# Kernel optimization log

Measured on AMD Instinct MI355X. Metric: run time of the kernel, lower is better.

Reference implementation:

```python
import jax, jax.numpy as jnp
import numpy as np

H = 8            # num_heads
SIM_THRESH = 0.75


def setup_inputs() -> dict:
    key = jax.random.key(0)
    ks = jax.random.split(key, 6)
    B, N, C, CR = 1, 1536, 256, 64
    x_cls = jax.random.normal(ks[0], (B, N, C), dtype=jnp.float32)
    x_reg = jax.random.normal(ks[1], (B, N, CR), dtype=jnp.float32)
    cls_score = jax.random.uniform(ks[2], (N,), dtype=jnp.float32)
    fg_score = jax.random.uniform(ks[3], (1, 1, 1, N), dtype=jnp.float32)
    W_cls = jax.random.normal(ks[4], (C, 3 * C), dtype=jnp.float32) / np.sqrt(C).astype(np.float32)
    W_reg = jax.random.normal(ks[5], (CR, 3 * CR), dtype=jnp.float32) / np.sqrt(CR).astype(np.float32)
    return {"x_cls": x_cls, "x_reg": x_reg, "cls_score": cls_score,
            "fg_score": fg_score, "W_cls": W_cls, "W_reg": W_reg}


def _l2norm(t):
    return t / jnp.linalg.norm(t, axis=-1, keepdims=True)


def _split_qkv(x, W):
    B, N, C = x.shape
    qkv = (x @ W).reshape(B, N, 3, H, C // H).transpose(2, 0, 3, 1, 4)  # [3,B,H,N,hd]
    return qkv[0], qkv[1], qkv[2]


def reference(x_cls, x_reg, cls_score, fg_score, W_cls, W_reg):
    B, N, C = x_cls.shape
    CR = x_reg.shape[-1]
    scale = (C // H) ** -0.5  # note: torch code uses the cls head_dim scale for BOTH branches

    q, k, v = _split_qkv(x_cls, W_cls)
    qn, kn, vn = _l2norm(q), _l2norm(k), _l2norm(v)
    qr, kr, vr = _split_qkv(x_reg, W_reg)
    qrn, krn, vrn = _l2norm(qr), _l2norm(kr), _l2norm(vr)

    # cls_score broadcast: value cls_score[j] at position (i, j), as in torch's reshape+repeat
    cs = cls_score.reshape(1, 1, 1, N)
    cls_mask = (cs > jnp.swapaxes(cs, -2, -1) - 0.1).astype(jnp.float32)        # [1,1,N,N]
    fg_mask = (fg_score > jnp.swapaxes(fg_score, -2, -1) - 0.1).astype(jnp.float32)  # [1,1,N,N]

    # raw cosine-similarity matrices of the (normalized) value vectors
    attn_cls_raw = jnp.einsum('bhid,bhjd->bhij', vn, vn)   # [B,H,N,N]
    attn_reg_raw = jnp.einsum('bhid,bhjd->bhij', vrn, vrn)

    attn_cls = jax.nn.softmax(
        jnp.einsum('bhid,bhjd->bhij', qn, kn) * scale * cs * cls_mask, axis=-1)
    attn_reg = jax.nn.softmax(
        jnp.einsum('bhid,bhjd->bhij', qrn, krn) * scale, axis=-1)
    attn = (attn_cls + attn_reg) * 0.5

    # threshold masks (mask=True, use_mask=True, sim_thresh=0.75 defaults)
    sim_mask = (attn_cls_raw.mean(axis=1) > SIM_THRESH).astype(jnp.float32)    # [B,N,N]
    sim_mask = jnp.broadcast_to(sim_mask[:, None], (B, H, N, N))
    sim_mask = sim_mask * cls_mask[0, 0] * fg_mask[0, 0]
    obj_mask = (attn_reg_raw.mean(axis=1)[0] > SIM_THRESH).astype(jnp.float32)  # [N,N]

    attn = sim_mask * attn
    obj_mask = obj_mask * sim_mask                                   # [B,H,N,N]
    obj_mask = obj_mask / jnp.sum(obj_mask, axis=-1, keepdims=True)  # safe: diagonal always 1
    attn = obj_mask * attn

    x = jnp.einsum('bhij,bhjd->bhid', attn, v).transpose(0, 2, 1, 3).reshape(B, N, C)
    out_cls = jnp.concatenate([x, x_cls], axis=-1)                   # [B,N,2C]
    xr = jnp.einsum('bhij,bhjd->bhid', attn, vr).transpose(0, 2, 1, 3).reshape(B, N, CR)
    out_reg = jnp.concatenate([xr, x_reg], axis=-1)                  # [B,N,2*CR]
    return out_cls, out_reg, sim_mask, obj_mask
```

## Files before the change

kernel.cpp:

```cpp
#include <hip/hip_runtime.h>
#include <hip/hip_bf16.h>

#define NT 1536
#define SCALE 0.17677669529663687f

typedef __attribute__((ext_vector_type(8))) short bf16x8;
typedef __attribute__((ext_vector_type(4))) float f32x4;

static __device__ __forceinline__ unsigned short f2b(float x) {
    __hip_bfloat16 h = __float2bfloat16(x);
    union { __hip_bfloat16 b; unsigned short u; } cv; cv.b = h; return cv.u;
}
static __device__ __forceinline__ float b2f(unsigned short u) {
    union { float f; unsigned v; } c; c.v = ((unsigned)u) << 16; return c.f;
}

__global__ __launch_bounds__(256) void prep(
    const float* __restrict__ x_cls, const float* __restrict__ x_reg,
    const float* __restrict__ W_cls, const float* __restrict__ W_reg,
    unsigned short* __restrict__ xb_c, unsigned short* __restrict__ xb_r,
    unsigned short* __restrict__ Wt_c, unsigned short* __restrict__ Wt_r)
{
    const int u = blockIdx.x * 256 + threadIdx.x;
    if (u < 393216) {
        xb_c[u] = f2b(x_cls[u]);
    } else if (u < 491520) {
        const int v = u - 393216;
        xb_r[v] = f2b(x_reg[v]);
    } else if (u < 688128) {
        const int v = u - 491520;
        const int j = v >> 8, k = v & 255;
        Wt_c[v] = f2b(W_cls[k * 768 + j]);
    } else if (u < 700416) {
        const int v = u - 688128;
        const int j = v >> 6, k = v & 63;
        Wt_r[v] = f2b(W_reg[k * 192 + j]);
    }
}

__global__ __launch_bounds__(256) void gemm_mfma(
    const unsigned short* __restrict__ xb_c, const unsigned short* __restrict__ Wt_c,
    const unsigned short* __restrict__ xb_r, const unsigned short* __restrict__ Wt_r,
    float* __restrict__ qkv_c, unsigned short* __restrict__ qb_c,
    float* __restrict__ qkv_r, unsigned short* __restrict__ qb_r)
{
    const unsigned short *A, *B;
    float* qkv; unsigned short* qb;
    int K, NN, KS;
    const bool isreg = (blockIdx.z == 1);
    if (!isreg) { A = xb_c; B = Wt_c; qkv = qkv_c; qb = qb_c; K = 256; NN = 768; KS = 8; }
    else { if (blockIdx.x >= 3) return;
           A = xb_r; B = Wt_r; qkv = qkv_r; qb = qb_r; K = 64;  NN = 192; KS = 2; }
    __shared__ short Ai[64 * 40], Bj[64 * 40];
    const int t = threadIdx.x, lane = t & 63;
    const int wv = t >> 6, wr = wv >> 1, wc = wv & 1;
    const int i0 = blockIdx.y * 64, j0 = blockIdx.x * 64;
    const int srow = t >> 2, sc8 = (t & 3) * 8;
    f32x4 acc[2][2];
    #pragma unroll
    for (int a = 0; a < 2; a++)
        #pragma unroll
        for (int b = 0; b < 2; b++) acc[a][b] = (f32x4){0, 0, 0, 0};
    float4 ra = *(const float4*)&A[(i0 + srow) * K + 0 * 32 + sc8];
    float4 rb = *(const float4*)&B[(j0 + srow) * K + 0 * 32 + sc8];
    float4 ra2, rb2;
    if (KS > 1) {
        ra2 = *(const float4*)&A[(i0 + srow) * K + 1 * 32 + sc8];
        rb2 = *(const float4*)&B[(j0 + srow) * K + 1 * 32 + sc8];
    }
    for (int ks = 0; ks < KS; ks++) {
        __syncthreads();
        *(float4*)&Ai[srow * 40 + sc8] = ra;
        *(float4*)&Bj[srow * 40 + sc8] = rb;
        ra = ra2; rb = rb2;
        if (ks + 2 < KS) {
            ra2 = *(const float4*)&A[(i0 + srow) * K + (ks + 2) * 32 + sc8];
            rb2 = *(const float4*)&B[(j0 + srow) * K + (ks + 2) * 32 + sc8];
        }
        __syncthreads();
        const int k8 = (lane >> 4) * 8;
        bf16x8 af[2], bf_[2];
        #pragma unroll
        for (int fr = 0; fr < 2; fr++)
            af[fr] = *(const bf16x8*)&Ai[(wr * 32 + fr * 16 + (lane & 15)) * 40 + k8];
        #pragma unroll
        for (int fc = 0; fc < 2; fc++)
            bf_[fc] = *(const bf16x8*)&Bj[(wc * 32 + fc * 16 + (lane & 15)) * 40 + k8];
        #pragma unroll
        for (int fr = 0; fr < 2; fr++)
            #pragma unroll
            for (int fc = 0; fc < 2; fc++)
                acc[fr][fc] = __builtin_amdgcn_mfma_f32_16x16x32_bf16(af[fr], bf_[fc], acc[fr][fc], 0, 0, 0);
    }
    #pragma unroll
    for (int fr = 0; fr < 2; fr++)
        #pragma unroll
        for (int r4 = 0; r4 < 4; r4++) {
            const int i = i0 + wr * 32 + fr * 16 + (lane >> 4) * 4 + r4;
            if (!isreg) {
                float s = acc[fr][0][r4] * acc[fr][0][r4] + acc[fr][1][r4] * acc[fr][1][r4];
                s += __shfl_xor(s, 1); s += __shfl_xor(s, 2);
                s += __shfl_xor(s, 4); s += __shfl_xor(s, 8);
                const float inv = 1.0f / sqrtf(s);
                #pragma unroll
                for (int fc = 0; fc < 2; fc++) {
                    const int j = j0 + wc * 32 + fc * 16 + (lane & 15);
                    const float v = acc[fr][fc][r4];
                    qkv[i * NN + j] = v;
                    qb[i * NN + j] = f2b(v * inv);
                }
            } else {
                #pragma unroll
                for (int fc = 0; fc < 2; fc++) {
                    const float v = acc[fr][fc][r4];
                    float s = v * v;
                    s += __shfl_xor(s, 1); s += __shfl_xor(s, 2); s += __shfl_xor(s, 4);
                    const float inv = 1.0f / sqrtf(s);
                    const int j = j0 + wc * 32 + fc * 16 + (lane & 15);
                    qkv[i * NN + j] = v;
                    qb[i * NN + j] = f2b(v * inv);
                }
            }
        }
}

__global__ __launch_bounds__(256) void bitsdenom(
    const unsigned short* __restrict__ qb_cls, const unsigned short* __restrict__ qb_reg,
    const float* __restrict__ cls_score, const float* __restrict__ fg_score,
    unsigned* __restrict__ simbits, unsigned* __restrict__ objbits,
    float* __restrict__ Dcpart, float* __restrict__ Drpart)
{
    __shared__ short Ai[64 * 40], Bj[64 * 40];
    __shared__ short Kr[64 * 72], Qr[64 * 72];
    __shared__ float csi[64], csj[64], fgi[64], fgj[64];
    __shared__ unsigned simw[64][2], objw[64][2];
    const int t = threadIdx.x;
    const int lane = t & 63;
    const int wv = t >> 6, wr = wv >> 1, wc = wv & 1;
    const int sr = t >> 2, sc = t & 3;

    if (blockIdx.x < 576) {
        const int iB = blockIdx.x / 24, jB = blockIdx.x % 24;
        const int i0 = iB * 64, j0 = jB * 64;
        if (t < 64)       { csi[t] = cls_score[i0 + t]; fgi[t] = fg_score[i0 + t]; }
        else if (t < 128) { csj[t - 64] = cls_score[j0 + t - 64]; fgj[t - 64] = fg_score[j0 + t - 64]; }
        f32x4 ac[2][2], ar[2][2];
        #pragma unroll
        for (int a = 0; a < 2; a++)
            #pragma unroll
            for (int b = 0; b < 2; b++) { ac[a][b] = (f32x4){0,0,0,0}; ar[a][b] = (f32x4){0,0,0,0}; }
        #define LD_A(s) ((s) < 8 ? *(const float4*)&qb_cls[(i0 + sr) * 768 + 512 + (s) * 32 + sc * 8] \
                                 : *(const float4*)&qb_reg[(i0 + sr) * 192 + 128 + ((s) - 8) * 32 + sc * 8])
        #define LD_B(s) ((s) < 8 ? *(const float4*)&qb_cls[(j0 + sr) * 768 + 512 + (s) * 32 + sc * 8] \
                                 : *(const float4*)&qb_reg[(j0 + sr) * 192 + 128 + ((s) - 8) * 32 + sc * 8])
        float4 ra = LD_A(0), rb = LD_B(0);
        float4 ra2 = LD_A(1), rb2 = LD_B(1);
        for (int ks = 0; ks < 10; ks++) {
            __syncthreads();
            *(float4*)&Ai[sr * 40 + sc * 8] = ra;
            *(float4*)&Bj[sr * 40 + sc * 8] = rb;
            ra = ra2; rb = rb2;
            if (ks + 2 < 10) { ra2 = LD_A(ks + 2); rb2 = LD_B(ks + 2); }
            __syncthreads();
            const int k8 = (lane >> 4) * 8;
            bf16x8 af[2], bf_[2];
            #pragma unroll
            for (int fr = 0; fr < 2; fr++)
                af[fr] = *(const bf16x8*)&Ai[(wr * 32 + fr * 16 + (lane & 15)) * 40 + k8];
            #pragma unroll
            for (int fc = 0; fc < 2; fc++)
                bf_[fc] = *(const bf16x8*)&Bj[(wc * 32 + fc * 16 + (lane & 15)) * 40 + k8];
            if (ks < 8) {
                #pragma unroll
                for (int fr = 0; fr < 2; fr++)
                    #pragma unroll
                    for (int fc = 0; fc < 2; fc++)
                        ac[fr][fc] = __builtin_amdgcn_mfma_f32_16x16x32_bf16(af[fr], bf_[fc], ac[fr][fc], 0, 0, 0);
            } else {
                #pragma unroll
                for (int fr = 0; fr < 2; fr++)
                    #pragma unroll
                    for (int fc = 0; fc < 2; fc++)
                        ar[fr][fc] = __builtin_amdgcn_mfma_f32_16x16x32_bf16(af[fr], bf_[fc], ar[fr][fc], 0, 0, 0);
            }
        }
        #undef LD_A
        #undef LD_B
        #pragma unroll
        for (int fr = 0; fr < 2; fr++)
            #pragma unroll
            for (int r4 = 0; r4 < 4; r4++) {
                const int rloc = wr * 32 + fr * 16 + (lane >> 4) * 4 + r4;
                const float ci = csi[rloc] - 0.1f, fgv = fgi[rloc] - 0.1f;
                unsigned sm[2], om[2];
                #pragma unroll
                for (int fc = 0; fc < 2; fc++) {
                    const int cloc = wc * 32 + fc * 16 + (lane & 15);
                    const bool clsb = csj[cloc] > ci;
                    const bool fgb  = fgj[cloc] > fgv;
                    const bool sim = (ac[fr][fc][r4] * 0.125f > 0.75f) && clsb && fgb;
                    const bool obj = sim && (ar[fr][fc][r4] * 0.125f > 0.75f);
                    unsigned long long bs = __ballot(sim);
                    unsigned long long bo = __ballot(obj);
                    const int g = lane >> 4;
                    sm[fc] = (unsigned)((bs >> (16 * g)) & 0xFFFFull);
                    om[fc] = (unsigned)((bo >> (16 * g)) & 0xFFFFull);
                }
                if ((lane & 15) == 0) {
                    simw[rloc][wc] = sm[0] | (sm[1] << 16);
                    objw[rloc][wc] = om[0] | (om[1] << 16);
                }
            }
        __syncthreads();
        if (t < 128) {
            const int row = t >> 1, w = t & 1;
            simbits[(i0 + row) * 48 + jB * 2 + w] = simw[row][w];
            objbits[(i0 + row) * 48 + jB * 2 + w] = objw[row][w];
        }
    } else {
        const int vd = blockIdx.x - 576;
        const int iB = vd / 24, jB = vd % 24;
        const int i0 = iB * 64, j0 = jB * 64;
        if (t < 64)       csj[t] = cls_score[j0 + t];
        else if (t < 128) csi[t - 64] = cls_score[i0 + t - 64];
        #pragma unroll
        for (int it = 0; it < 2; it++) {
            const int u = it * 256 + t;
            const int r = u >> 3, c = u & 7;
            *(float4*)&Kr[r * 72 + c * 8] = *(const float4*)&qb_reg[(j0 + r) * 192 + 64 + c * 8];
            *(float4*)&Qr[r * 72 + c * 8] = *(const float4*)&qb_reg[(i0 + r) * 192 + 0 + c * 8];
        }
        __syncthreads();
        float cI[2], cJ[8];
        #pragma unroll
        for (int fc = 0; fc < 2; fc++) cI[fc] = csi[wc * 32 + fc * 16 + (lane & 15)] - 0.1f;
        #pragma unroll
        for (int fr = 0; fr < 2; fr++)
            #pragma unroll
            for (int r4 = 0; r4 < 4; r4++)
                cJ[fr * 4 + r4] = csj[wr * 32 + fr * 16 + (lane >> 4) * 4 + r4];
        float pC[2][8], pR[2][8];
        const bool g0 = (lane >> 4) == 0;
        const bf16x8 zz = {0, 0, 0, 0, 0, 0, 0, 0};
        float4 ra = *(const float4*)&qb_cls[(j0 + sr) * 768 + 256 + 0 * 32 + sc * 8];
        float4 rb = *(const float4*)&qb_cls[(i0 + sr) * 768 + 0   + 0 * 32 + sc * 8];
        float4 ra2 = *(const float4*)&qb_cls[(j0 + sr) * 768 + 256 + 1 * 32 + sc * 8];
        float4 rb2 = *(const float4*)&qb_cls[(i0 + sr) * 768 + 0   + 1 * 32 + sc * 8];
        for (int h = 0; h < 8; h++) {
            __syncthreads();
            *(float4*)&Ai[sr * 40 + sc * 8] = ra;
            *(float4*)&Bj[sr * 40 + sc * 8] = rb;
            ra = ra2; rb = rb2;
            if (h + 2 < 8) {
                ra2 = *(const float4*)&qb_cls[(j0 + sr) * 768 + 256 + (h + 2) * 32 + sc * 8];
                rb2 = *(const float4*)&qb_cls[(i0 + sr) * 768 + 0   + (h + 2) * 32 + sc * 8];
            }
            __syncthreads();
            const int k8 = (lane >> 4) * 8;
            bf16x8 a[2], b[2], arg[2], brg[2];
            #pragma unroll
            for (int fr = 0; fr < 2; fr++) {
                const int row = wr * 32 + fr * 16 + (lane & 15);
                a[fr] = *(const bf16x8*)&Ai[row * 40 + k8];
                arg[fr] = g0 ? *(const bf16x8*)&Kr[row * 72 + h * 8] : zz;
            }
            #pragma unroll
            for (int fc = 0; fc < 2; fc++) {
                const int row = wc * 32 + fc * 16 + (lane & 15);
                b[fc] = *(const bf16x8*)&Bj[row * 40 + k8];
                brg[fc] = g0 ? *(const bf16x8*)&Qr[row * 72 + h * 8] : zz;
            }
            f32x4 acc[2][2], racc[2][2];
            #pragma unroll
            for (int fr = 0; fr < 2; fr++)
                #pragma unroll
                for (int fc = 0; fc < 2; fc++) {
                    acc[fr][fc] = (f32x4){0,0,0,0};
                    racc[fr][fc] = (f32x4){0,0,0,0};
                    acc[fr][fc] = __builtin_amdgcn_mfma_f32_16x16x32_bf16(a[fr], b[fc], acc[fr][fc], 0, 0, 0);
                    racc[fr][fc] = __builtin_amdgcn_mfma_f32_16x16x32_bf16(arg[fr], brg[fc], racc[fr][fc], 0, 0, 0);
                }
            #pragma unroll
            for (int fc = 0; fc < 2; fc++) {
                float sC = 0.f, sR = 0.f;
                #pragma unroll
                for (int fr = 0; fr < 2; fr++)
                    #pragma unroll
                    for (int r4 = 0; r4 < 4; r4++) {
                        const float cj = cJ[fr * 4 + r4];
                        const float lc = (cj > cI[fc]) ? acc[fr][fc][r4] * SCALE * cj : 0.0f;
                        sC += __expf(lc);
                        sR += __expf(racc[fr][fc][r4] * SCALE);
                    }
                pC[fc][h] = sC; pR[fc][h] = sR;
            }
        }
        #pragma unroll
        for (int fc = 0; fc < 2; fc++)
            #pragma unroll
            for (int h = 0; h < 8; h++) {
                float v = pC[fc][h]; v += __shfl_xor(v, 16); v += __shfl_xor(v, 32);
                float u = pR[fc][h]; u += __shfl_xor(u, 16); u += __shfl_xor(u, 32);
                if (lane < 16) {
                    const int i = i0 + wc * 32 + fc * 16 + lane;
                    const int p = jB * 2 + wr;
                    Dcpart[(p * NT + i) * 8 + h] = v;
                    Drpart[(p * NT + i) * 8 + h] = u;
                }
            }
    }
}

__global__ __launch_bounds__(256) void finish(
    const float* __restrict__ qkv_cls, const unsigned short* __restrict__ qb_cls,
    const float* __restrict__ qkv_reg, const unsigned short* __restrict__ qb_reg,
    const float* __restrict__ cls_score,
    const unsigned* __restrict__ simbits, const unsigned* __restrict__ objbits,
    const float* __restrict__ Dcpart, const float* __restrict__ Drpart,
    const float* __restrict__ x_cls, const float* __restrict__ x_reg,
    float* __restrict__ out_cls, float* __restrict__ out_reg,
    float* __restrict__ sim_out, float* __restrict__ obj_out)
{
    __shared__ unsigned bw[6][48];
    __shared__ float invs[6];
    const int t = threadIdx.x;
    if (blockIdx.x < 384) {
        const int i = (blockIdx.x << 2) + (t >> 6);
        const int l = t & 63;
        const int g = l >> 3;
        const ushort4 qu = *(const ushort4*)&qb_cls[i * 768 + 4 * l];
        const float qx = b2f(qu.x), qy = b2f(qu.y), qz = b2f(qu.z), qw = b2f(qu.w);
        const float qr = b2f(qb_reg[i * 192 + l]);
        unsigned myw = (l < 48) ? objbits[i * 48 + l] : 0u;
        int cnt = __popc(myw);
        #pragma unroll
        for (int m = 1; m < 64; m <<= 1) cnt += __shfl_xor(cnt, m);
        const int s = l & 7;
        float Dcv = 0.f, Drv = 0.f;
        #pragma unroll
        for (int p6 = 0; p6 < 6; p6++) {
            const int p = s * 6 + p6;
            Dcv += Dcpart[(p * NT + i) * 8 + g];
            Drv += Drpart[(p * NT + i) * 8 + g];
        }
        Dcv += __shfl_xor(Dcv, 1); Dcv += __shfl_xor(Dcv, 2); Dcv += __shfl_xor(Dcv, 4);
        Drv += __shfl_xor(Drv, 1); Drv += __shfl_xor(Drv, 2); Drv += __shfl_xor(Drv, 4);
        float a1x = 0.f, a1y = 0.f, a1z = 0.f, a1w = 0.f;
        float a2x = 0.f, a2y = 0.f, a2z = 0.f, a2w = 0.f;
        float rr1 = 0.f, rr2 = 0.f;
        for (int w = 0; w < 48; w++) {
            unsigned bits = __shfl(myw, w);
            while (bits) {
                const int b = __ffs(bits) - 1;
                bits &= bits - 1u;
                const int j = w * 32 + b;
                const ushort4 ku = *(const ushort4*)&qb_cls[j * 768 + 256 + 4 * l];
                const float4 v4 = *(const float4*)&qkv_cls[j * 768 + 512 + 4 * l];
                const float kr = b2f(qb_reg[j * 192 + 64 + l]);
                const float vr = qkv_reg[j * 192 + 128 + l];
                float dc = qx * b2f(ku.x) + qy * b2f(ku.y) + qz * b2f(ku.z) + qw * b2f(ku.w);
                dc += __shfl_xor(dc, 1); dc += __shfl_xor(dc, 2); dc += __shfl_xor(dc, 4);
                float dr = qr * kr;
                dr += __shfl_xor(dr, 1); dr += __shfl_xor(dr, 2); dr += __shfl_xor(dr, 4);
                const float cj = cls_score[j];
                const float ec = __expf(dc * SCALE * cj);
                const float er = __expf(dr * SCALE);
                a1x += ec * v4.x; a1y += ec * v4.y; a1z += ec * v4.z; a1w += ec * v4.w;
                a2x += er * v4.x; a2y += er * v4.y; a2z += er * v4.z; a2w += er * v4.w;
                rr1 += ec * vr;   rr2 += er * vr;
            }
        }
        const float iDc = 1.0f / Dcv, iDr = 1.0f / Drv;
        const float hi = 0.5f / (float)cnt;
        float4 o;
        o.x = (a1x * iDc + a2x * iDr) * hi;
        o.y = (a1y * iDc + a2y * iDr) * hi;
        o.z = (a1z * iDc + a2z * iDr) * hi;
        o.w = (a1w * iDc + a2w * iDr) * hi;
        *(float4*)&out_cls[i * 512 + 4 * l] = o;
        out_reg[i * 128 + l] = (rr1 * iDc + rr2 * iDr) * hi;
        *(float4*)&out_cls[i * 512 + 256 + 4 * l] = *(const float4*)&x_cls[i * 256 + 4 * l];
        out_reg[i * 128 + 64 + l] = x_reg[i * 64 + l];
    } else {
        const int eb = blockIdx.x - 384;
        const int arr = eb >> 11;
        const int rem = eb & 2047;
        const int copy = rem >> 8;
        const int blk = rem & 255;
        const int r0 = blk * 6;
        const unsigned* src = arr ? objbits : simbits;
        for (int u = t; u < 288; u += 256) bw[u / 48][u % 48] = src[(r0 + u / 48) * 48 + (u % 48)];
        __syncthreads();
        if (t < 6) {
            int c = 0;
            #pragma unroll 8
            for (int w = 0; w < 48; w++) c += __popc(bw[t][w]);
            invs[t] = 1.0f / (float)c;
        }
        __syncthreads();
        f32x4* dst = (f32x4*)((arr ? obj_out : sim_out)
                              + (size_t)copy * NT * NT + (size_t)r0 * NT);
        #pragma unroll
        for (int rpt = 0; rpt < 9; rpt++) {
            const int u = rpt * 256 + t;
            const int row = u / 384;
            const int c4 = u - row * 384;
            const int j0 = c4 * 4;
            const unsigned w = bw[row][j0 >> 5] >> (j0 & 31);
            const float on = arr ? invs[row] : 1.0f;
            f32x4 v;
            v.x = (w & 1u) ? on : 0.f;
            v.y = (w & 2u) ? on : 0.f;
            v.z = (w & 4u) ? on : 0.f;
            v.w = (w & 8u) ? on : 0.f;
            __builtin_nontemporal_store(v, dst + u);
        }
    }
}

extern "C" void kernel_launch(void* const* d_in, const int* in_sizes, int n_in,
                              void* d_out, int out_size, void* d_ws, size_t ws_size,
                              hipStream_t stream)
{
    (void)in_sizes; (void)n_in; (void)out_size; (void)ws_size;
    const float* x_cls     = (const float*)d_in[0];
    const float* x_reg     = (const float*)d_in[1];
    const float* cls_score = (const float*)d_in[2];
    const float* fg_score  = (const float*)d_in[3];
    const float* W_cls     = (const float*)d_in[4];
    const float* W_reg     = (const float*)d_in[5];

    float* out = (float*)d_out;
    float* out_cls = out;
    float* out_reg = out + 786432;
    float* sim_out = out + 983040;
    float* obj_out = out + 19857408;

    float* wsf = (float*)d_ws;
    float* qkv_cls = wsf;
    float* qkv_reg = wsf + 1179648;
    float* Dcpart  = wsf + 1474560;
    float* Drpart  = wsf + 2064384;
    unsigned short* qb_cls = (unsigned short*)(wsf + 2654208);
    unsigned short* qb_reg = (unsigned short*)(wsf + 3244032);
    unsigned short* xb_c   = (unsigned short*)(wsf + 3391488);
    unsigned short* xb_r   = (unsigned short*)(wsf + 3588096);
    unsigned short* Wt_c   = (unsigned short*)(wsf + 3637248);
    unsigned short* Wt_r   = (unsigned short*)(wsf + 3735552);
    unsigned* simbits = (unsigned*)(wsf + 3741696);
    unsigned* objbits = simbits + 73728;

    prep<<<2736, 256, 0, stream>>>(x_cls, x_reg, W_cls, W_reg, xb_c, xb_r, Wt_c, Wt_r);
    gemm_mfma<<<dim3(12, 24, 2), 256, 0, stream>>>(
        xb_c, Wt_c, xb_r, Wt_r, qkv_cls, qb_cls, qkv_reg, qb_reg);
    bitsdenom<<<1152, 256, 0, stream>>>(
        qb_cls, qb_reg, cls_score, fg_score, simbits, objbits, Dcpart, Drpart);
    finish<<<4480, 256, 0, stream>>>(
        qkv_cls, qb_cls, qkv_reg, qb_reg, cls_score,
        simbits, objbits, Dcpart, Drpart, x_cls, x_reg,
        out_cls, out_reg, sim_out, obj_out);
}
```

Measured before the change: 81.84 us.

## Regroup kernels so denominator blocks interleave with mask expansion stores

Splits the bitmask MFMA pass into its own kernel. The softmax-denominator blocks now share a launch with the large sim/obj mask expansion, interleaved one denominator block per seven expansion blocks, and the sparse attention output moves to a separate final kernel. The intent is to overlap the compute-bound denominator work with the store-bound writing of the 2x8xNxN masks instead of running them in separate phases. It adds one kernel launch and makes the denominator blocks depend on the masks being finished.

Measured after the change: 169.9 us. 108% more time.

```diff
diff --git a/kernel.cpp b/kernel.cpp
--- a/kernel.cpp
+++ b/kernel.cpp
@@ -124,103 +124,119 @@
         }
 }
 
-__global__ __launch_bounds__(256) void bitsdenom(
+__global__ __launch_bounds__(256) void bits_mfma(
     const unsigned short* __restrict__ qb_cls, const unsigned short* __restrict__ qb_reg,
     const float* __restrict__ cls_score, const float* __restrict__ fg_score,
-    unsigned* __restrict__ simbits, unsigned* __restrict__ objbits,
-    float* __restrict__ Dcpart, float* __restrict__ Drpart)
+    unsigned* __restrict__ simbits, unsigned* __restrict__ objbits)
 {
     __shared__ short Ai[64 * 40], Bj[64 * 40];
-    __shared__ short Kr[64 * 72], Qr[64 * 72];
     __shared__ float csi[64], csj[64], fgi[64], fgj[64];
     __shared__ unsigned simw[64][2], objw[64][2];
     const int t = threadIdx.x;
     const int lane = t & 63;
     const int wv = t >> 6, wr = wv >> 1, wc = wv & 1;
     const int sr = t >> 2, sc = t & 3;
-
-    if (blockIdx.x < 576) {
-        const int iB = blockIdx.x / 24, jB = blockIdx.x % 24;
+    const int iB = blockIdx.x / 24, jB = blockIdx.x % 24;
+    const int i0 = iB * 64, j0 = jB * 64;
+    if (t < 64)       { csi[t] = cls_score[i0 + t]; fgi[t] = fg_score[i0 + t]; }
+    else if (t < 128) { csj[t - 64] = cls_score[j0 + t - 64]; fgj[t - 64] = fg_score[j0 + t - 64]; }
+    f32x4 ac[2][2], ar[2][2];
+    #pragma unroll
+    for (int a = 0; a < 2; a++)
+        #pragma unroll
+        for (int b = 0; b < 2; b++) { ac[a][b] = (f32x4){0,0,0,0}; ar[a][b] = (f32x4){0,0,0,0}; }
+    #define LD_A(s) ((s) < 8 ? *(const float4*)&qb_cls[(i0 + sr) * 768 + 512 + (s) * 32 + sc * 8] \
+                             : *(const float4*)&qb_reg[(i0 + sr) * 192 + 128 + ((s) - 8) * 32 + sc * 8])
+    #define LD_B(s) ((s) < 8 ? *(const float4*)&qb_cls[(j0 + sr) * 768 + 512 + (s) * 32 + sc * 8] \
+                             : *(const float4*)&qb_reg[(j0 + sr) * 192 + 128 + ((s) - 8) * 32 + sc * 8])
+    float4 ra = LD_A(0), rb = LD_B(0);
+    float4 ra2 = LD_A(1), rb2 = LD_B(1);
+    for (int ks = 0; ks < 10; ks++) {
+        __syncthreads();
+        *(float4*)&Ai[sr * 40 + sc * 8] = ra;
+        *(float4*)&Bj[sr * 40 + sc * 8] = rb;
+        ra = ra2; rb = rb2;
+        if (ks + 2 < 10) { ra2 = LD_A(ks + 2); rb2 = LD_B(ks + 2); }
+        __syncthreads();
+        const int k8 = (lane >> 4) * 8;
+        bf16x8 af[2], bf_[2];
+        #pragma unroll
+        for (int fr = 0; fr < 2; fr++)
+            af[fr] = *(const bf16x8*)&Ai[(wr * 32 + fr * 16 + (lane & 15)) * 40 + k8];
+        #pragma unroll
+        for (int fc = 0; fc < 2; fc++)
+            bf_[fc] = *(const bf16x8*)&Bj[(wc * 32 + fc * 16 + (lane & 15)) * 40 + k8];
+        if (ks < 8) {
+            #pragma unroll
+            for (int fr = 0; fr < 2; fr++)
+                #pragma unroll
+                for (int fc = 0; fc < 2; fc++)
+                    ac[fr][fc] = __builtin_amdgcn_mfma_f32_16x16x32_bf16(af[fr], bf_[fc], ac[fr][fc], 0, 0, 0);
+        } else {
+            #pragma unroll
+            for (int fr = 0; fr < 2; fr++)
+                #pragma unroll
+                for (int fc = 0; fc < 2; fc++)
+                    ar[fr][fc] = __builtin_amdgcn_mfma_f32_16x16x32_bf16(af[fr], bf_[fc], ar[fr][fc], 0, 0, 0);
+        }
+    }
+    #undef LD_A
+    #undef LD_B
+    #pragma unroll
+    for (int fr = 0; fr < 2; fr++)
+        #pragma unroll
+        for (int r4 = 0; r4 < 4; r4++) {
+            const int rloc = wr * 32 + fr * 16 + (lane >> 4) * 4 + r4;
+            const float ci = csi[rloc] - 0.1f, fgv = fgi[rloc] - 0.1f;
+            unsigned sm[2], om[2];
+            #pragma unroll
+            for (int fc = 0; fc < 2; fc++) {
+                const int cloc = wc * 32 + fc * 16 + (lane & 15);
+                const bool clsb = csj[cloc] > ci;
+                const bool fgb  = fgj[cloc] > fgv;
+                const bool sim = (ac[fr][fc][r4] * 0.125f > 0.75f) && clsb && fgb;
+                const bool obj = sim && (ar[fr][fc][r4] * 0.125f > 0.75f);
+                unsigned long long bs = __ballot(sim);
+                unsigned long long bo = __ballot(obj);
+                const int g = lane >> 4;
+                sm[fc] = (unsigned)((bs >> (16 * g)) & 0xFFFFull);
+                om[fc] = (unsigned)((bo >> (16 * g)) & 0xFFFFull);
+            }
+            if ((lane & 15) == 0) {
+                simw[rloc][wc] = sm[0] | (sm[1] << 16);
+                objw[rloc][wc] = om[0] | (om[1] << 16);
+            }
+        }
+    __syncthreads();
+    if (t < 128) {
+        const int row = t >> 1, w = t & 1;
+        simbits[(i0 + row) * 48 + jB * 2 + w] = simw[row][w];
+        objbits[(i0 + row) * 48 + jB * 2 + w] = objw[row][w];
+    }
+}
+
+__global__ __launch_bounds__(256) void denomexpand(
+    const unsigned short* __restrict__ qb_cls, const unsigned short* __restrict__ qb_reg,
+    const float* __restrict__ cls_score,
+    const unsigned* __restrict__ simbits, const unsigned* __restrict__ objbits,
+    float* __restrict__ Dcpart, float* __restrict__ Drpart,
+    float* __restrict__ sim_out, float* __restrict__ obj_out)
+{
+    __shared__ short Ai[64 * 40], Bj[64 * 40];
+    __shared__ short Kr[64 * 72], Qr[64 * 72];
+    __shared__ float csi[64], csj[64];
+    __shared__ unsigned bw[6][48];
+    __shared__ float invs[6];
+    const int t = threadIdx.x;
+    const int bid = blockIdx.x;
+    if ((bid & 7) == 7) {
+        const int didx = bid >> 3;
+        if (didx >= 576) return;
+        const int iB = didx / 24, jB = didx % 24;
         const int i0 = iB * 64, j0 = jB * 64;
-        if (t < 64)       { csi[t] = cls_score[i0 + t]; fgi[t] = fg_score[i0 + t]; }
-        else if (t < 128) { csj[t - 64] = cls_score[j0 + t - 64]; fgj[t - 64] = fg_score[j0 + t - 64]; }
-        f32x4 ac[2][2], ar[2][2];
-        #pragma unroll
-        for (int a = 0; a < 2; a++)
-            #pragma unroll
-            for (int b = 0; b < 2; b++) { ac[a][b] = (f32x4){0,0,0,0}; ar[a][b] = (f32x4){0,0,0,0}; }
-        #define LD_A(s) ((s) < 8 ? *(const float4*)&qb_cls[(i0 + sr) * 768 + 512 + (s) * 32 + sc * 8] \
-                                 : *(const float4*)&qb_reg[(i0 + sr) * 192 + 128 + ((s) - 8) * 32 + sc * 8])
-        #define LD_B(s) ((s) < 8 ? *(const float4*)&qb_cls[(j0 + sr) * 768 + 512 + (s) * 32 + sc * 8] \
-                                 : *(const float4*)&qb_reg[(j0 + sr) * 192 + 128 + ((s) - 8) * 32 + sc * 8])
-        float4 ra = LD_A(0), rb = LD_B(0);
-        float4 ra2 = LD_A(1), rb2 = LD_B(1);
-        for (int ks = 0; ks < 10; ks++) {
-            __syncthreads();
-            *(float4*)&Ai[sr * 40 + sc * 8] = ra;
-            *(float4*)&Bj[sr * 40 + sc * 8] = rb;
-            ra = ra2; rb = rb2;
-            if (ks + 2 < 10) { ra2 = LD_A(ks + 2); rb2 = LD_B(ks + 2); }
-            __syncthreads();
-            const int k8 = (lane >> 4) * 8;
-            bf16x8 af[2], bf_[2];
-            #pragma unroll
-            for (int fr = 0; fr < 2; fr++)
-                af[fr] = *(const bf16x8*)&Ai[(wr * 32 + fr * 16 + (lane & 15)) * 40 + k8];
-            #pragma unroll
-            for (int fc = 0; fc < 2; fc++)
-                bf_[fc] = *(const bf16x8*)&Bj[(wc * 32 + fc * 16 + (lane & 15)) * 40 + k8];
-            if (ks < 8) {
-                #pragma unroll
-                for (int fr = 0; fr < 2; fr++)
-                    #pragma unroll
-                    for (int fc = 0; fc < 2; fc++)
-                        ac[fr][fc] = __builtin_amdgcn_mfma_f32_16x16x32_bf16(af[fr], bf_[fc], ac[fr][fc], 0, 0, 0);
-            } else {
-                #pragma unroll
-                for (int fr = 0; fr < 2; fr++)
-                    #pragma unroll
-                    for (int fc = 0; fc < 2; fc++)
-                        ar[fr][fc] = __builtin_amdgcn_mfma_f32_16x16x32_bf16(af[fr], bf_[fc], ar[fr][fc], 0, 0, 0);
-            }
-        }
-        #undef LD_A
-        #undef LD_B
-        #pragma unroll
-        for (int fr = 0; fr < 2; fr++)
-            #pragma unroll
-            for (int r4 = 0; r4 < 4; r4++) {
-                const int rloc = wr * 32 + fr * 16 + (lane >> 4) * 4 + r4;
-                const float ci = csi[rloc] - 0.1f, fgv = fgi[rloc] - 0.1f;
-                unsigned sm[2], om[2];
-                #pragma unroll
-                for (int fc = 0; fc < 2; fc++) {
-                    const int cloc = wc * 32 + fc * 16 + (lane & 15);
-                    const bool clsb = csj[cloc] > ci;
-                    const bool fgb  = fgj[cloc] > fgv;
-                    const bool sim = (ac[fr][fc][r4] * 0.125f > 0.75f) && clsb && fgb;
-                    const bool obj = sim && (ar[fr][fc][r4] * 0.125f > 0.75f);
-                    unsigned long long bs = __ballot(sim);
-                    unsigned long long bo = __ballot(obj);
-                    const int g = lane >> 4;
-                    sm[fc] = (unsigned)((bs >> (16 * g)) & 0xFFFFull);
-                    om[fc] = (unsigned)((bo >> (16 * g)) & 0xFFFFull);
-                }
-                if ((lane & 15) == 0) {
-                    simw[rloc][wc] = sm[0] | (sm[1] << 16);
-                    objw[rloc][wc] = om[0] | (om[1] << 16);
-                }
-            }
-        __syncthreads();
-        if (t < 128) {
-            const int row = t >> 1, w = t & 1;
-            simbits[(i0 + row) * 48 + jB * 2 + w] = simw[row][w];
-            objbits[(i0 + row) * 48 + jB * 2 + w] = objw[row][w];
-        }
-    } else {
-        const int vd = blockIdx.x - 576;
-        const int iB = vd / 24, jB = vd % 24;
-        const int i0 = iB * 64, j0 = jB * 64;
+        const int lane = t & 63;
+        const int wv = t >> 6, wr = wv >> 1, wc = wv & 1;
+        const int sr = t >> 2, sc = t & 3;
         if (t < 64)       csj[t] = cls_score[j0 + t];
         else if (t < 128) csi[t - 64] = cls_score[i0 + t - 64];
         #pragma unroll
@@ -308,83 +324,11 @@
                     Drpart[(p * NT + i) * 8 + h] = u;
                 }
             }
-    }
-}
-
-__global__ __launch_bounds__(256) void finish(
-    const float* __restrict__ qkv_cls, const unsigned short* __restrict__ qb_cls,
-    const float* __restrict__ qkv_reg, const unsigned short* __restrict__ qb_reg,
-    const float* __restrict__ cls_score,
-    const unsigned* __restrict__ simbits, const unsigned* __restrict__ objbits,
-    const float* __restrict__ Dcpart, const float* __restrict__ Drpart,
-    const float* __restrict__ x_cls, const float* __restrict__ x_reg,
-    float* __restrict__ out_cls, float* __restrict__ out_reg,
-    float* __restrict__ sim_out, float* __restrict__ obj_out)
-{
-    __shared__ unsigned bw[6][48];
-    __shared__ float invs[6];
-    const int t = threadIdx.x;
-    if (blockIdx.x < 384) {
-        const int i = (blockIdx.x << 2) + (t >> 6);
-        const int l = t & 63;
-        const int g = l >> 3;
-        const ushort4 qu = *(const ushort4*)&qb_cls[i * 768 + 4 * l];
-        const float qx = b2f(qu.x), qy = b2f(qu.y), qz = b2f(qu.z), qw = b2f(qu.w);
-        const float qr = b2f(qb_reg[i * 192 + l]);
-        unsigned myw = (l < 48) ? objbits[i * 48 + l] : 0u;
-        int cnt = __popc(myw);
-        #pragma unroll
-        for (int m = 1; m < 64; m <<= 1) cnt += __shfl_xor(cnt, m);
-        const int s = l & 7;
-        float Dcv = 0.f, Drv = 0.f;
-        #pragma unroll
-        for (int p6 = 0; p6 < 6; p6++) {
-            const int p = s * 6 + p6;
-            Dcv += Dcpart[(p * NT + i) * 8 + g];
-            Drv += Drpart[(p * NT + i) * 8 + g];
-        }
-        Dcv += __shfl_xor(Dcv, 1); Dcv += __shfl_xor(Dcv, 2); Dcv += __shfl_xor(Dcv, 4);
-        Drv += __shfl_xor(Drv, 1); Drv += __shfl_xor(Drv, 2); Drv += __shfl_xor(Drv, 4);
-        float a1x = 0.f, a1y = 0.f, a1z = 0.f, a1w = 0.f;
-        float a2x = 0.f, a2y = 0.f, a2z = 0.f, a2w = 0.f;
-        float rr1 = 0.f, rr2 = 0.f;
-        for (int w = 0; w < 48; w++) {
-            unsigned bits = __shfl(myw, w);
-            while (bits) {
-                const int b = __ffs(bits) - 1;
-                bits &= bits - 1u;
-                const int j = w * 32 + b;
-                const ushort4 ku = *(const ushort4*)&qb_cls[j * 768 + 256 + 4 * l];
-                const float4 v4 = *(const float4*)&qkv_cls[j * 768 + 512 + 4 * l];
-                const float kr = b2f(qb_reg[j * 192 + 64 + l]);
-                const float vr = qkv_reg[j * 192 + 128 + l];
-                float dc = qx * b2f(ku.x) + qy * b2f(ku.y) + qz * b2f(ku.z) + qw * b2f(ku.w);
-                dc += __shfl_xor(dc, 1); dc += __shfl_xor(dc, 2); dc += __shfl_xor(dc, 4);
-                float dr = qr * kr;
-                dr += __shfl_xor(dr, 1); dr += __shfl_xor(dr, 2); dr += __shfl_xor(dr, 4);
-                const float cj = cls_score[j];
-                const float ec = __expf(dc * SCALE * cj);
-                const float er = __expf(dr * SCALE);
-                a1x += ec * v4.x; a1y += ec * v4.y; a1z += ec * v4.z; a1w += ec * v4.w;
-                a2x += er * v4.x; a2y += er * v4.y; a2z += er * v4.z; a2w += er * v4.w;
-                rr1 += ec * vr;   rr2 += er * vr;
-            }
-        }
-        const float iDc = 1.0f / Dcv, iDr = 1.0f / Drv;
-        const float hi = 0.5f / (float)cnt;
-        float4 o;
-        o.x = (a1x * iDc + a2x * iDr) * hi;
-        o.y = (a1y * iDc + a2y * iDr) * hi;
-        o.z = (a1z * iDc + a2z * iDr) * hi;
-        o.w = (a1w * iDc + a2w * iDr) * hi;
-        *(float4*)&out_cls[i * 512 + 4 * l] = o;
-        out_reg[i * 128 + l] = (rr1 * iDc + rr2 * iDr) * hi;
-        *(float4*)&out_cls[i * 512 + 256 + 4 * l] = *(const float4*)&x_cls[i * 256 + 4 * l];
-        out_reg[i * 128 + 64 + l] = x_reg[i * 64 + l];
     } else {
-        const int eb = blockIdx.x - 384;
-        const int arr = eb >> 11;
-        const int rem = eb & 2047;
+        const int eidx = (bid >> 3) * 7 + (bid & 7);
+        if (eidx >= 4096) return;
+        const int arr = eidx >> 11;
+        const int rem = eidx & 2047;
         const int copy = rem >> 8;
         const int blk = rem & 255;
         const int r0 = blk * 6;
@@ -418,6 +362,73 @@
     }
 }
 
+__global__ __launch_bounds__(256) void out_small(
+    const float* __restrict__ qkv_cls, const unsigned short* __restrict__ qb_cls,
+    const float* __restrict__ qkv_reg, const unsigned short* __restrict__ qb_reg,
+    const float* __restrict__ cls_score,
+    const unsigned* __restrict__ objbits,
+    const float* __restrict__ Dcpart, const float* __restrict__ Drpart,
+    const float* __restrict__ x_cls, const float* __restrict__ x_reg,
+    float* __restrict__ out_cls, float* __restrict__ out_reg)
+{
+    const int i = (blockIdx.x << 2) + (threadIdx.x >> 6);
+    const int l = threadIdx.x & 63;
+    const int g = l >> 3;
+    const ushort4 qu = *(const ushort4*)&qb_cls[i * 768 + 4 * l];
+    const float qx = b2f(qu.x), qy = b2f(qu.y), qz = b2f(qu.z), qw = b2f(qu.w);
+    const float qr = b2f(qb_reg[i * 192 + l]);
+    unsigned myw = (l < 48) ? objbits[i * 48 + l] : 0u;
+    int cnt = __popc(myw);
+    #pragma unroll
+    for (int m = 1; m < 64; m <<= 1) cnt += __shfl_xor(cnt, m);
+    const int s = l & 7;
+    float Dcv = 0.f, Drv = 0.f;
+    #pragma unroll
+    for (int p6 = 0; p6 < 6; p6++) {
+        const int p = s * 6 + p6;
+        Dcv += Dcpart[(p * NT + i) * 8 + g];
+        Drv += Drpart[(p * NT + i) * 8 + g];
+    }
+    Dcv += __shfl_xor(Dcv, 1); Dcv += __shfl_xor(Dcv, 2); Dcv += __shfl_xor(Dcv, 4);
+    Drv += __shfl_xor(Drv, 1); Drv += __shfl_xor(Drv, 2); Drv += __shfl_xor(Drv, 4);
+    float a1x = 0.f, a1y = 0.f, a1z = 0.f, a1w = 0.f;
+    float a2x = 0.f, a2y = 0.f, a2z = 0.f, a2w = 0.f;
+    float rr1 = 0.f, rr2 = 0.f;
+    for (int w = 0; w < 48; w++) {
+        unsigned bits = __shfl(myw, w);
+        while (bits) {
+            const int b = __ffs(bits) - 1;
+            bits &= bits - 1u;
+            const int j = w * 32 + b;
+            const ushort4 ku = *(const ushort4*)&qb_cls[j * 768 + 256 + 4 * l];
+            const float4 v4 = *(const float4*)&qkv_cls[j * 768 + 512 + 4 * l];
+            const float kr = b2f(qb_reg[j * 192 + 64 + l]);
+            const float vr = qkv_reg[j * 192 + 128 + l];
+            float dc = qx * b2f(ku.x) + qy * b2f(ku.y) + qz * b2f(ku.z) + qw * b2f(ku.w);
+            dc += __shfl_xor(dc, 1); dc += __shfl_xor(dc, 2); dc += __shfl_xor(dc, 4);
+            float dr = qr * kr;
+            dr += __shfl_xor(dr, 1); dr += __shfl_xor(dr, 2); dr += __shfl_xor(dr, 4);
+            const float cj = cls_score[j];
+            const float ec = __expf(dc * SCALE * cj);
+            const float er = __expf(dr * SCALE);
+            a1x += ec * v4.x; a1y += ec * v4.y; a1z += ec * v4.z; a1w += ec * v4.w;
+            a2x += er * v4.x; a2y += er * v4.y; a2z += er * v4.z; a2w += er * v4.w;
+            rr1 += ec * vr;   rr2 += er * vr;
+        }
+    }
+    const float iDc = 1.0f / Dcv, iDr = 1.0f / Drv;
+    const float hi = 0.5f / (float)cnt;
+    float4 o;
+    o.x = (a1x * iDc + a2x * iDr) * hi;
+    o.y = (a1y * iDc + a2y * iDr) * hi;
+    o.z = (a1z * iDc + a2z * iDr) * hi;
+    o.w = (a1w * iDc + a2w * iDr) * hi;
+    *(float4*)&out_cls[i * 512 + 4 * l] = o;
+    out_reg[i * 128 + l] = (rr1 * iDc + rr2 * iDr) * hi;
+    *(float4*)&out_cls[i * 512 + 256 + 4 * l] = *(const float4*)&x_cls[i * 256 + 4 * l];
+    out_reg[i * 128 + 64 + l] = x_reg[i * 64 + l];
+}
+
 extern "C" void kernel_launch(void* const* d_in, const int* in_sizes, int n_in,
                               void* d_out, int out_size, void* d_ws, size_t ws_size,
                               hipStream_t stream)
@@ -453,10 +464,12 @@
     prep<<<2736, 256, 0, stream>>>(x_cls, x_reg, W_cls, W_reg, xb_c, xb_r, Wt_c, Wt_r);
     gemm_mfma<<<dim3(12, 24, 2), 256, 0, stream>>>(
         xb_c, Wt_c, xb_r, Wt_r, qkv_cls, qb_cls, qkv_reg, qb_reg);
-    bitsdenom<<<1152, 256, 0, stream>>>(
-        qb_cls, qb_reg, cls_score, fg_score, simbits, objbits, Dcpart, Drpart);
-    finish<<<4480, 256, 0, stream>>>(
+    bits_mfma<<<576, 256, 0, stream>>>(
+        qb_cls, qb_reg, cls_score, fg_score, simbits, objbits);
+    denomexpand<<<4688, 256, 0, stream>>>(
+        qb_cls, qb_reg, cls_score, simbits, objbits,
+        Dcpart, Drpart, sim_out, obj_out);
+    out_small<<<384, 256, 0, stream>>>(
         qkv_cls, qb_cls, qkv_reg, qb_reg, cls_score,
-        simbits, objbits, Dcpart, Drpart, x_cls, x_reg,
-        out_cls, out_reg, sim_out, obj_out);
-}
+        objbits, Dcpart, Drpart, x_cls, x_reg, out_cls, out_reg);
+}
```
